# Kernel tuning notes

Hardware: AMD Instinct MI355X
Metric: run time of the kernel (lower is better)

The kernel has to match this reference:

```python
import jax, jax.numpy as jnp
import numpy as np

N = 4096          # in_features
M = 4096          # out_features
RANK = 64
FT = 16           # ft_rank (trainable LoRA)
RES = RANK - FT   # frozen low-rank residual
CB = 65536        # E8P: 16-bit codeword per group of 8 weights
CW = 8            # codeword width (E8 lattice dim)
Q_SCALE = 0.02
GLOBAL_SCALE = 1.0


def _hadamard(n):
    # Sylvester construction, normalized: H @ H.T = I (matches matmul_hadU/hadUt up to transpose; H is symmetric)
    H = np.array([[1.0]], dtype=np.float32)
    while H.shape[0] < n:
        H = np.block([[H, H], [H, -H]])
    return H / np.sqrt(np.float32(n))


def setup_inputs() -> dict:
    key = jax.random.key(0)
    ks = jax.random.split(key, 9)
    x = jax.random.normal(ks[0], (8192, N), jnp.float32)
    Q_idxs = jax.random.randint(ks[1], (M, N // CW), 0, CB, dtype=jnp.int32)
    grid = jax.random.normal(ks[2], (CB, CW), jnp.float32) * 0.5   # E8P codebook grid
    SU = jax.random.rademacher(ks[3], (N,), dtype=jnp.float32)     # random sign vectors (QuIP#)
    SV = jax.random.rademacher(ks[4], (M,), dtype=jnp.float32)
    L_ft = jax.random.normal(ks[5], (M, FT), jnp.float32) * 0.02
    R_ft = jax.random.normal(ks[6], (FT, N), jnp.float32) * 0.02
    L_res = jax.random.normal(ks[7], (M, RES), jnp.float32) * 0.02
    R_res = jax.random.normal(ks[8], (RES, N), jnp.float32) * 0.02
    had_left = jnp.asarray(_hadamard(N))
    had_right = jnp.asarray(_hadamard(M))
    return {"x": x, "SU": SU, "SV": SV, "grid": grid, "L_ft": L_ft, "R_ft": R_ft,
            "L_res": L_res, "R_res": R_res, "had_left": had_left,
            "had_right": had_right, "Q_idxs": Q_idxs}


def reference(x, SU, SV, grid, L_ft, R_ft, L_res, R_res, had_left, had_right, Q_idxs):
    shape = x.shape
    h = x.reshape(-1, N) * SU                 # x * SU
    h = h @ had_left                          # matmul_hadUt (Hadamard is symmetric orthogonal)
    # E8P codebook decode: gather 8-dim codewords -> full [M, N] weight, fused matmul
    W = grid[Q_idxs].reshape(M, N)            # [M, N//8, 8] -> [M, N]
    out = (h @ W.T) * Q_SCALE                 # Q.forward
    out = out + (h @ R_res.T) @ L_res.T       # frozen low-rank residual (rank - ft_rank)
    out = out + (h @ R_ft.T) @ L_ft.T         # trainable LoRA path
    out = (out @ had_right) * GLOBAL_SCALE    # matmul_hadU * global_scale
    out = out * SV
    return out.reshape(*shape[:-1], M)
```

## Files before the change

### kernel.cpp

```cpp
#include <hip/hip_runtime.h>
#include <hip/hip_bf16.h>
#include <stdint.h>


typedef __bf16 bf16;
typedef __bf16 bf16x8 __attribute__((ext_vector_type(8)));
typedef float f32x4 __attribute__((ext_vector_type(4)));

#define KE 4160
#define NN 4096
#define MM 4096
#define BB 8192

__global__ void prep_kernel(const float* __restrict__ Lft, const float* __restrict__ Rft,
                            const float* __restrict__ Lres, const float* __restrict__ Rres,
                            bf16* __restrict__ Rcat, bf16* __restrict__ Wq) {
  int tid = blockIdx.x * 256 + threadIdx.x;
  if (tid < 64 * 4096) {
    int r = tid >> 12, n = tid & 4095;
    float v = (r < 48) ? Rres[r * 4096 + n] : Rft[(r - 48) * 4096 + n];
    Rcat[tid] = (bf16)v;
  } else {
    int t2 = tid - 64 * 4096;
    int m = t2 >> 6, r = t2 & 63;
    float v = (r < 48) ? Lres[m * 48 + r] : Lft[m * 16 + (r - 48)];
    Wq[(size_t)m * KE + 4096 + r] = (bf16)v;
  }
}

__global__ void decode_kernel(const int* __restrict__ qidx, const float* __restrict__ grid,
                              bf16* __restrict__ Wq) {
  int tid = blockIdx.x * 256 + threadIdx.x;
  int m = tid >> 9, g = tid & 511;
  uint32_t idx = (uint32_t)qidx[tid];
  const float4* gp = (const float4*)(grid + (size_t)idx * 8);
  float4 w0 = gp[0], w1 = gp[1];
  bf16x8 o;
  o[0] = (bf16)(w0.x * 0.02f); o[1] = (bf16)(w0.y * 0.02f);
  o[2] = (bf16)(w0.z * 0.02f); o[3] = (bf16)(w0.w * 0.02f);
  o[4] = (bf16)(w1.x * 0.02f); o[5] = (bf16)(w1.y * 0.02f);
  o[6] = (bf16)(w1.z * 0.02f); o[7] = (bf16)(w1.w * 0.02f);
  *(bf16x8*)(Wq + (size_t)m * KE + g * 8) = o;
}

#define SK(i) ((i) + ((i) >> 5))

__global__ void fwht_pre_kernel(const float* __restrict__ src,
                                bf16* __restrict__ dst,
                                const float* __restrict__ SU) {
  __shared__ float buf[4224];
  const int row = blockIdx.x, t = threadIdx.x;
  const float4* sp = (const float4*)(src + (size_t)row * NN + t * 16);
  const float4* su = (const float4*)(SU + t * 16);
  float v[16];
#pragma unroll
  for (int q = 0; q < 4; ++q) {
    float4 a = sp[q], s = su[q];
    v[q * 4 + 0] = a.x * s.x; v[q * 4 + 1] = a.y * s.y;
    v[q * 4 + 2] = a.z * s.z; v[q * 4 + 3] = a.w * s.w;
  }
#pragma unroll
  for (int s = 1; s < 16; s <<= 1) {
#pragma unroll
    for (int i = 0; i < 16; ++i) {
      if (!(i & s)) { float a = v[i], b = v[i + s]; v[i] = a + b; v[i + s] = a - b; }
    }
  }
#pragma unroll
  for (int i = 0; i < 16; ++i) buf[SK(t * 16 + i)] = v[i];
  for (int s = 16; s < 4096; s <<= 1) {
    __syncthreads();
#pragma unroll
    for (int j = 0; j < 8; ++j) {
      int p = t + j * 256;
      int i = ((p & ~(s - 1)) << 1) | (p & (s - 1));
      float a = buf[SK(i)], b = buf[SK(i + s)];
      buf[SK(i)] = a + b; buf[SK(i + s)] = a - b;
    }
  }
  __syncthreads();
  bf16x8 o0, o1;
#pragma unroll
  for (int i = 0; i < 8; ++i) {
    o0[i] = (bf16)(buf[SK(t * 16 + i)] * 0.015625f);
    o1[i] = (bf16)(buf[SK(t * 16 + 8 + i)] * 0.015625f);
  }
  bf16* dp = dst + (size_t)row * KE + t * 16;
  *(bf16x8*)dp = o0;
  *(bf16x8*)(dp + 8) = o1;
}

__global__ void fwht_post_kernel(float* __restrict__ data, const float* __restrict__ SV) {
  __shared__ float buf[4224];
  const int row = blockIdx.x, t = threadIdx.x;
  float4* dp = (float4*)(data + (size_t)row * MM + t * 16);
  float v[16];
#pragma unroll
  for (int q = 0; q < 4; ++q) {
    float4 a = dp[q];
    v[q * 4 + 0] = a.x; v[q * 4 + 1] = a.y; v[q * 4 + 2] = a.z; v[q * 4 + 3] = a.w;
  }
#pragma unroll
  for (int s = 1; s < 16; s <<= 1) {
#pragma unroll
    for (int i = 0; i < 16; ++i) {
      if (!(i & s)) { float a = v[i], b = v[i + s]; v[i] = a + b; v[i + s] = a - b; }
    }
  }
#pragma unroll
  for (int i = 0; i < 16; ++i) buf[SK(t * 16 + i)] = v[i];
  for (int s = 16; s < 4096; s <<= 1) {
    __syncthreads();
#pragma unroll
    for (int j = 0; j < 8; ++j) {
      int p = t + j * 256;
      int i = ((p & ~(s - 1)) << 1) | (p & (s - 1));
      float a = buf[SK(i)], b = buf[SK(i + s)];
      buf[SK(i)] = a + b; buf[SK(i + s)] = a - b;
    }
  }
  __syncthreads();
  const float4* sv = (const float4*)(SV + t * 16);
#pragma unroll
  for (int q = 0; q < 4; ++q) {
    float4 s = sv[q];
    float4 o;
    o.x = buf[SK(t * 16 + q * 4 + 0)] * 0.015625f * s.x;
    o.y = buf[SK(t * 16 + q * 4 + 1)] * 0.015625f * s.y;
    o.z = buf[SK(t * 16 + q * 4 + 2)] * 0.015625f * s.z;
    o.w = buf[SK(t * 16 + q * 4 + 3)] * 0.015625f * s.w;
    dp[q] = o;
  }
}

__global__ void __launch_bounds__(256) tgemm_kernel(const bf16* __restrict__ A,
                                                    const bf16* __restrict__ Bm,
                                                    float* __restrict__ Tpart) {
  __shared__ bf16 lA[128 * 32];
  __shared__ bf16 lB[64 * 32];
  const int t = threadIdx.x, w = t >> 6, l = t & 63;
  const int bmBlk = blockIdx.x;
  const int split = blockIdx.y;
  const int wm = w >> 1, wn = w & 1;
  f32x4 acc[4][2] = {};
  const int arow = t >> 1, acol = (t & 1) * 16;
  const bf16* pa = A + (size_t)(bmBlk * 128 + arow) * KE + acol;
  const int brow = (t & 127) >> 1, bcol = acol;
  const bf16* pb = Bm + (size_t)brow * 4096 + bcol;
  const int fr = l & 15, fk = (l >> 4) * 8;
  for (int kt = 0; kt < 32; ++kt) {
    const int k0 = (split * 32 + kt) * 32;
    bf16x8 a0 = *(const bf16x8*)(pa + k0);
    bf16x8 a1 = *(const bf16x8*)(pa + k0 + 8);
    *(bf16x8*)&lA[arow * 32 + acol] = a0;
    *(bf16x8*)&lA[arow * 32 + acol + 8] = a1;
    if (t < 128) {
      bf16x8 b0 = *(const bf16x8*)(pb + k0);
      bf16x8 b1 = *(const bf16x8*)(pb + k0 + 8);
      *(bf16x8*)&lB[brow * 32 + bcol] = b0;
      *(bf16x8*)&lB[brow * 32 + bcol + 8] = b1;
    }
    __syncthreads();
    bf16x8 af[4], bfr[2];
#pragma unroll
    for (int i = 0; i < 4; ++i) af[i] = *(const bf16x8*)&lA[(wm * 64 + i * 16 + fr) * 32 + fk];
#pragma unroll
    for (int i = 0; i < 2; ++i) bfr[i] = *(const bf16x8*)&lB[(wn * 32 + i * 16 + fr) * 32 + fk];
#pragma unroll
    for (int mi = 0; mi < 4; ++mi)
#pragma unroll
      for (int ni = 0; ni < 2; ++ni)
        acc[mi][ni] = __builtin_amdgcn_mfma_f32_16x16x32_bf16(af[mi], bfr[ni], acc[mi][ni], 0, 0, 0);
    __syncthreads();
  }
  float* out = Tpart + (size_t)split * BB * 64;
  const int orow = bmBlk * 128 + wm * 64 + (l >> 4) * 4;
  const int ocol = wn * 32 + (l & 15);
#pragma unroll
  for (int mi = 0; mi < 4; ++mi)
#pragma unroll
    for (int ni = 0; ni < 2; ++ni)
#pragma unroll
      for (int r = 0; r < 4; ++r)
        out[(size_t)(orow + mi * 16 + r) * 64 + ocol + ni * 16] = acc[mi][ni][r];
}

__global__ void tconv_kernel(const float* __restrict__ Tpart, bf16* __restrict__ h) {
  int i = blockIdx.x * 256 + threadIdx.x;
  float s = Tpart[i] + Tpart[i + BB * 64] + Tpart[i + 2 * BB * 64] + Tpart[i + 3 * BB * 64];
  int row = i >> 6, c = i & 63;
  h[(size_t)row * KE + 4096 + c] = (bf16)s;
}


__device__ __forceinline__ void gload16(const void* g, void* l) {
  __builtin_amdgcn_global_load_lds(
      (const __attribute__((address_space(1))) void*)g,
      (__attribute__((address_space(3))) void*)l, 16, 0, 0);
}

__device__ __forceinline__ void bar() {
  asm volatile("" ::: "memory");
  __builtin_amdgcn_s_barrier();
  asm volatile("" ::: "memory");
}

__global__ void __launch_bounds__(512, 2) mgemm_kernel(const bf16* __restrict__ A,
                                                       const bf16* __restrict__ B,
                                                       float* __restrict__ C) {
  __shared__ alignas(16) char sA[65536];
  __shared__ alignas(16) char sB[65536];
  const int t = threadIdx.x;
  const int w = t >> 6, l = t & 63;
  const int wm = w >> 2, wn = w & 3;
  const int bid = blockIdx.x;
  const int swzb = (bid & 7) * 64 + (bid >> 3);
  const int bm = swzb >> 4, bn = swzb & 15;

  const int c0 = w * 2, c1 = w * 2 + 1;
  const int lb0 = c0 * 1024 + l * 16;
  const int lb1 = c1 * 1024 + l * 16;
  const int sb0 = lb0 ^ (((lb0 >> 7) & 3) << 4);
  const int sb1 = lb1 ^ (((lb1 >> 7) & 3) << 4);
  const char* gA0 = (const char*)(A + (size_t)(bm * 256 + (sb0 >> 6)) * KE) + (sb0 & 63);
  const char* gA1 = (const char*)(A + (size_t)(bm * 256 + (sb1 >> 6)) * KE) + (sb1 & 63);
  const char* gB0 = (const char*)(B + (size_t)(bn * 256 + (sb0 >> 6)) * KE) + (sb0 & 63);
  const char* gB1 = (const char*)(B + (size_t)(bn * 256 + (sb1 >> 6)) * KE) + (sb1 & 63);

  const int fr = l & 15, fkb = (l >> 4) * 16;
  int offA[8], offB[4];
#pragma unroll
  for (int mi = 0; mi < 8; ++mi) {
    int lb = (wm * 128 + mi * 16 + fr) * 64 + fkb;
    offA[mi] = lb ^ (((lb >> 7) & 3) << 4);
  }
#pragma unroll
  for (int ni = 0; ni < 4; ++ni) {
    int lb = (wn * 64 + ni * 16 + fr) * 64 + fkb;
    offB[ni] = lb ^ (((lb >> 7) & 3) << 4);
  }

  f32x4 acc[8][4] = {};

#pragma unroll
  for (int p = 0; p < 3; ++p) {
    gload16(gA0 + (size_t)p * 64, &sA[p * 16384 + c0 * 1024]);
    gload16(gA1 + (size_t)p * 64, &sA[p * 16384 + c1 * 1024]);
    gload16(gB0 + (size_t)p * 64, &sB[p * 16384 + c0 * 1024]);
    gload16(gB1 + (size_t)p * 64, &sB[p * 16384 + c1 * 1024]);
  }
  asm volatile("s_waitcnt vmcnt(8)" ::: "memory");
  __builtin_amdgcn_sched_barrier(0);
  bar();

  for (int i = 0; i < 130; ++i) {
    const int sbs = (i & 3) << 14;
    const int s3b = ((i + 3) & 3) << 14;
    const size_t ko = (size_t)(i + 3) << 6;
    bf16x8 af[4], bv[4];
#pragma unroll
    for (int mi = 0; mi < 4; ++mi) af[mi] = *(const bf16x8*)&sA[sbs + offA[mi]];
#pragma unroll
    for (int ni = 0; ni < 4; ++ni) bv[ni] = *(const bf16x8*)&sB[sbs + offB[ni]];
    if (i < 127) {
      gload16(gA0 + ko, &sA[s3b + c0 * 1024]);
      gload16(gA1 + ko, &sA[s3b + c1 * 1024]);
    }
    bar();
    __builtin_amdgcn_s_setprio(1);
#pragma unroll
    for (int mi = 0; mi < 4; ++mi)
#pragma unroll
      for (int ni = 0; ni < 4; ++ni)
        acc[mi][ni] = __builtin_amdgcn_mfma_f32_16x16x32_bf16(af[mi], bv[ni], acc[mi][ni], 0, 0, 0);
    __builtin_amdgcn_s_setprio(0);
    bar();
#pragma unroll
    for (int mi = 0; mi < 4; ++mi) af[mi] = *(const bf16x8*)&sA[sbs + offA[4 + mi]];
    if (i < 127) {
      gload16(gB0 + ko, &sB[s3b + c0 * 1024]);
      gload16(gB1 + ko, &sB[s3b + c1 * 1024]);
      asm volatile("s_waitcnt vmcnt(8)" ::: "memory");
      __builtin_amdgcn_sched_barrier(0);
    } else if (i == 127) {
      asm volatile("s_waitcnt vmcnt(4)" ::: "memory");
      __builtin_amdgcn_sched_barrier(0);
    } else if (i == 128) {
      asm volatile("s_waitcnt vmcnt(0)" ::: "memory");
      __builtin_amdgcn_sched_barrier(0);
    }
    bar();
    __builtin_amdgcn_s_setprio(1);
#pragma unroll
    for (int mi = 0; mi < 4; ++mi)
#pragma unroll
      for (int ni = 0; ni < 4; ++ni)
        acc[4 + mi][ni] = __builtin_amdgcn_mfma_f32_16x16x32_bf16(af[mi], bv[ni], acc[4 + mi][ni], 0, 0, 0);
    __builtin_amdgcn_s_setprio(0);
    bar();
  }

  const int orow = bm * 256 + wm * 128 + ((l >> 4) << 2);
  const int ocol = bn * 256 + wn * 64 + (l & 15);
#pragma unroll
  for (int mi = 0; mi < 8; ++mi)
#pragma unroll
    for (int ni = 0; ni < 4; ++ni)
#pragma unroll
      for (int r = 0; r < 4; ++r)
        C[(size_t)(orow + mi * 16 + r) * MM + ocol + ni * 16] = acc[mi][ni][r];
}

extern "C" void kernel_launch(void* const* d_in, const int* in_sizes, int n_in,
                              void* d_out, int out_size, void* d_ws, size_t ws_size,
                              hipStream_t stream) {
  const float* x    = (const float*)d_in[0];
  const float* SU   = (const float*)d_in[1];
  const float* SV   = (const float*)d_in[2];
  const float* grid = (const float*)d_in[3];
  const float* Lft  = (const float*)d_in[4];
  const float* Rft  = (const float*)d_in[5];
  const float* Lres = (const float*)d_in[6];
  const float* Rres = (const float*)d_in[7];
  const int*   qidx = (const int*)d_in[10];
  float* out = (float*)d_out;

  char* ws = (char*)d_ws;
  bf16*  h     = (bf16*)ws;
  bf16*  Wq    = (bf16*)(ws + 68157440);
  bf16*  Rcat  = (bf16*)(ws + 68157440 + 34078720);
  float* Tpart = (float*)(ws + 68157440 + 34078720 + 524288);

  prep_kernel<<<2048, 256, 0, stream>>>(Lft, Rft, Lres, Rres, Rcat, Wq);
  decode_kernel<<<8192, 256, 0, stream>>>(qidx, grid, Wq);
  fwht_pre_kernel<<<8192, 256, 0, stream>>>(x, h, SU);
  tgemm_kernel<<<dim3(64, 4), 256, 0, stream>>>(h, Rcat, Tpart);
  tconv_kernel<<<2048, 256, 0, stream>>>(Tpart, h);
  mgemm_kernel<<<512, 512, 0, stream>>>(h, Wq, out);
  fwht_post_kernel<<<8192, 256, 0, stream>>>(out, SV);
}
```

Baseline: 647.6 us.

## Drop FWHT LDS padding and prefetch second A fragment before first MFMA block

The Hadamard kernels stop using the padded LDS index (one pad word every 32 floats), which shrinks shared memory but may bring back bank conflicts at the butterfly strides. The main GEMM loop now loads all eight A fragments from LDS before the first MFMA group, instead of loading the second half between the two MFMA groups. This is meant to take the LDS read latency off the path between the two MFMA phases, at the cost of more VGPRs held live.

```diff
diff --git a/kernel.cpp b/kernel.cpp
--- a/kernel.cpp
+++ b/kernel.cpp
@@ -43,12 +43,10 @@
   *(bf16x8*)(Wq + (size_t)m * KE + g * 8) = o;
 }
 
-#define SK(i) ((i) + ((i) >> 5))
-
 __global__ void fwht_pre_kernel(const float* __restrict__ src,
                                 bf16* __restrict__ dst,
                                 const float* __restrict__ SU) {
-  __shared__ float buf[4224];
+  __shared__ float buf[4096];
   const int row = blockIdx.x, t = threadIdx.x;
   const float4* sp = (const float4*)(src + (size_t)row * NN + t * 16);
   const float4* su = (const float4*)(SU + t * 16);
@@ -67,23 +65,23 @@
     }
   }
 #pragma unroll
-  for (int i = 0; i < 16; ++i) buf[SK(t * 16 + i)] = v[i];
+  for (int i = 0; i < 16; ++i) buf[t * 16 + i] = v[i];
   for (int s = 16; s < 4096; s <<= 1) {
     __syncthreads();
 #pragma unroll
     for (int j = 0; j < 8; ++j) {
       int p = t + j * 256;
       int i = ((p & ~(s - 1)) << 1) | (p & (s - 1));
-      float a = buf[SK(i)], b = buf[SK(i + s)];
-      buf[SK(i)] = a + b; buf[SK(i + s)] = a - b;
+      float a = buf[i], b = buf[i + s];
+      buf[i] = a + b; buf[i + s] = a - b;
     }
   }
   __syncthreads();
   bf16x8 o0, o1;
 #pragma unroll
   for (int i = 0; i < 8; ++i) {
-    o0[i] = (bf16)(buf[SK(t * 16 + i)] * 0.015625f);
-    o1[i] = (bf16)(buf[SK(t * 16 + 8 + i)] * 0.015625f);
+    o0[i] = (bf16)(buf[t * 16 + i] * 0.015625f);
+    o1[i] = (bf16)(buf[t * 16 + 8 + i] * 0.015625f);
   }
   bf16* dp = dst + (size_t)row * KE + t * 16;
   *(bf16x8*)dp = o0;
@@ -91,7 +89,7 @@
 }
 
 __global__ void fwht_post_kernel(float* __restrict__ data, const float* __restrict__ SV) {
-  __shared__ float buf[4224];
+  __shared__ float buf[4096];
   const int row = blockIdx.x, t = threadIdx.x;
   float4* dp = (float4*)(data + (size_t)row * MM + t * 16);
   float v[16];
@@ -108,15 +106,15 @@
     }
   }
 #pragma unroll
-  for (int i = 0; i < 16; ++i) buf[SK(t * 16 + i)] = v[i];
+  for (int i = 0; i < 16; ++i) buf[t * 16 + i] = v[i];
   for (int s = 16; s < 4096; s <<= 1) {
     __syncthreads();
 #pragma unroll
     for (int j = 0; j < 8; ++j) {
       int p = t + j * 256;
       int i = ((p & ~(s - 1)) << 1) | (p & (s - 1));
-      float a = buf[SK(i)], b = buf[SK(i + s)];
-      buf[SK(i)] = a + b; buf[SK(i + s)] = a - b;
+      float a = buf[i], b = buf[i + s];
+      buf[i] = a + b; buf[i + s] = a - b;
     }
   }
   __syncthreads();
@@ -125,10 +123,10 @@
   for (int q = 0; q < 4; ++q) {
     float4 s = sv[q];
     float4 o;
-    o.x = buf[SK(t * 16 + q * 4 + 0)] * 0.015625f * s.x;
-    o.y = buf[SK(t * 16 + q * 4 + 1)] * 0.015625f * s.y;
-    o.z = buf[SK(t * 16 + q * 4 + 2)] * 0.015625f * s.z;
-    o.w = buf[SK(t * 16 + q * 4 + 3)] * 0.015625f * s.w;
+    o.x = buf[t * 16 + q * 4 + 0] * 0.015625f * s.x;
+    o.y = buf[t * 16 + q * 4 + 1] * 0.015625f * s.y;
+    o.z = buf[t * 16 + q * 4 + 2] * 0.015625f * s.z;
+    o.w = buf[t * 16 + q * 4 + 3] * 0.015625f * s.w;
     dp[q] = o;
   }
 }
@@ -257,11 +255,13 @@
     const int sbs = (i & 3) << 14;
     const int s3b = ((i + 3) & 3) << 14;
     const size_t ko = (size_t)(i + 3) << 6;
-    bf16x8 af[4], bv[4];
+    bf16x8 af[4], af2[4], bv[4];
 #pragma unroll
     for (int mi = 0; mi < 4; ++mi) af[mi] = *(const bf16x8*)&sA[sbs + offA[mi]];
 #pragma unroll
     for (int ni = 0; ni < 4; ++ni) bv[ni] = *(const bf16x8*)&sB[sbs + offB[ni]];
+#pragma unroll
+    for (int mi = 0; mi < 4; ++mi) af2[mi] = *(const bf16x8*)&sA[sbs + offA[4 + mi]];
     if (i < 127) {
       gload16(gA0 + ko, &sA[s3b + c0 * 1024]);
       gload16(gA1 + ko, &sA[s3b + c1 * 1024]);
@@ -275,8 +275,6 @@
         acc[mi][ni] = __builtin_amdgcn_mfma_f32_16x16x32_bf16(af[mi], bv[ni], acc[mi][ni], 0, 0, 0);
     __builtin_amdgcn_s_setprio(0);
     bar();
-#pragma unroll
-    for (int mi = 0; mi < 4; ++mi) af[mi] = *(const bf16x8*)&sA[sbs + offA[4 + mi]];
     if (i < 127) {
       gload16(gB0 + ko, &sB[s3b + c0 * 1024]);
       gload16(gB1 + ko, &sB[s3b + c1 * 1024]);
@@ -295,7 +293,7 @@
     for (int mi = 0; mi < 4; ++mi)
 #pragma unroll
       for (int ni = 0; ni < 4; ++ni)
-        acc[4 + mi][ni] = __builtin_amdgcn_mfma_f32_16x16x32_bf16(af[mi], bv[ni], acc[4 + mi][ni], 0, 0, 0);
+        acc[4 + mi][ni] = __builtin_amdgcn_mfma_f32_16x16x32_bf16(af2[mi], bv[ni], acc[4 + mi][ni], 0, 0, 0);
     __builtin_amdgcn_s_setprio(0);
     bar();
   }
```

After: 648.0 us. About the same (+0.1%).
